# Kernel optimization log

Measured on AMD Instinct MI355X. Metric: run time of the kernel, lower is better.

The kernel has to match this reference:

```python
import jax, jax.numpy as jnp
import numpy as np

B, C, H, W = 2, 64, 128, 128

def setup_inputs() -> dict:
    key = jax.random.key(0)
    k1, k2, k3 = jax.random.split(key, 3)
    x = jax.random.normal(k1, (B, C, H, W), dtype=jnp.float32)
    y = jax.random.normal(k2, (B, C, H, W), dtype=jnp.float32)
    z = jax.random.normal(k3, (B, C, H, W), dtype=jnp.float32)
    return {"x": x, "y": y, "z": z}

def reference(x, y, z):
    # x=q, y=k, z=v, all [b,c,h,w]. Per pixel:
    #   kv[i,j] = v[i] * k[j]          (c x c outer product)
    #   attn    = softmax over i (dim=1 in torch, the v axis)
    #   out[i]  = sum_j attn[i,j] * q[j]
    q = jnp.transpose(x, (0, 2, 3, 1))  # [b,h,w,c]
    k = jnp.transpose(y, (0, 2, 3, 1))
    v = jnp.transpose(z, (0, 2, 3, 1))
    kv = v[..., :, None] * k[..., None, :]          # [b,h,w,c,c]
    attn = jax.nn.softmax(kv, axis=-2)              # softmax over v-axis i
    out = jnp.einsum('bhwij,bhwj->bhwi', attn, q)   # [b,h,w,c]
    return jnp.transpose(out, (0, 3, 1, 2))         # [b,c,h,w]
```

## Files before the change

kernel.cpp:

```cpp
#include <hip/hip_runtime.h>


constexpr int C    = 64;
constexpr int HW   = 128 * 128;
constexpr int NPIX = 2 * HW;
constexpr int ICH  = 8;
constexpr int JT   = 8;
constexpr int LSTR = 68;
#define LOG2E 1.4426950408889634f

__device__ __forceinline__ float quad_xor1_add(float x) {
  int xi = __builtin_bit_cast(int, x);
  int yi = __builtin_amdgcn_update_dpp(0, xi, 0xB1, 0xF, 0xF, true);
  return x + __builtin_bit_cast(float, yi);
}
__device__ __forceinline__ float quad_xor2_add(float x) {
  int xi = __builtin_bit_cast(int, x);
  int yi = __builtin_amdgcn_update_dpp(0, xi, 0x4E, 0xF, 0xF, true);
  return x + __builtin_bit_cast(float, yi);
}
__device__ __forceinline__ float xor4_add(float x) {
  int xi = __builtin_bit_cast(int, x);
  int yi = __builtin_amdgcn_ds_swizzle(xi, 0x101F);
  return x + __builtin_bit_cast(float, yi);
}

__global__ __launch_bounds__(256, 4) void channel_mixing_kernel(
    const float* __restrict__ q,
    const float* __restrict__ kk,
    const float* __restrict__ v,
    float* __restrict__ out) {
  __shared__ __align__(16) float lds_k[32 * LSTR];
  __shared__ __align__(16) float lds_q[32 * LSTR];

  const int t        = threadIdx.x;
  const int pixblock = blockIdx.x * 32;
  const int gbase = ((pixblock >> 14) << 20) | (pixblock & (HW - 1));

#pragma unroll
  for (int rep = 0; rep < 8; ++rep) {
    const int idx = rep * 256 + t;
    const int j   = idx >> 5;
    const int px  = idx & 31;
    lds_k[px * LSTR + j] = kk[gbase + (j << 14) + px];
    lds_q[px * LSTR + j] = q [gbase + (j << 14) + px];
  }

  const int lane = t & 63;
  const int p    = lane >> 3;
  const int ig   = lane & 7;
  const int px   = (t >> 6) * 8 + p;
  const int base  = gbase + px;
  const int cbase = base + (ig << 17);

  float vv[ICH];
#pragma unroll
  for (int ii = 0; ii < ICH; ++ii)
    vv[ii] = v[cbase + (ii << 14)] * LOG2E;

  float acc[ICH];
#pragma unroll
  for (int ii = 0; ii < ICH; ++ii) acc[ii] = 0.0f;

  __syncthreads();

  const float* lkp = &lds_k[px * LSTR];
  const float* lqp = &lds_q[px * LSTR];

#pragma unroll 1
  for (int jt = 0; jt < C / JT; ++jt) {
    float kx[JT], qx[JT];
    *(float4*)&kx[0] = *(const float4*)&lkp[jt * JT];
    *(float4*)&kx[4] = *(const float4*)&lkp[jt * JT + 4];
    *(float4*)&qx[0] = *(const float4*)&lqp[jt * JT];
    *(float4*)&qx[4] = *(const float4*)&lqp[jt * JT + 4];

    float e[JT][ICH];
#pragma unroll
    for (int jj = 0; jj < JT; ++jj)
#pragma unroll
      for (int ii = 0; ii < ICH; ++ii)
        e[jj][ii] = __builtin_amdgcn_exp2f(vv[ii] * kx[jj]);

    float S[JT];
#pragma unroll
    for (int jj = 0; jj < JT; ++jj) {
      float s0 = (e[jj][0] + e[jj][1]) + (e[jj][2] + e[jj][3]);
      float s1 = (e[jj][4] + e[jj][5]) + (e[jj][6] + e[jj][7]);
      S[jj] = s0 + s1;
    }
#pragma unroll
    for (int jj = 0; jj < JT; ++jj) S[jj] = quad_xor1_add(S[jj]);
#pragma unroll
    for (int jj = 0; jj < JT; ++jj) S[jj] = quad_xor2_add(S[jj]);
#pragma unroll
    for (int jj = 0; jj < JT; ++jj) S[jj] = xor4_add(S[jj]);

#pragma unroll
    for (int jj = 0; jj < JT; ++jj) {
      const float w = qx[jj] * __builtin_amdgcn_rcpf(S[jj]);
#pragma unroll
      for (int ii = 0; ii < ICH; ++ii) acc[ii] += w * e[jj][ii];
    }
  }

#pragma unroll
  for (int ii = 0; ii < ICH; ++ii)
    out[cbase + (ii << 14)] = acc[ii];
}

extern "C" void kernel_launch(void* const* d_in, const int* in_sizes, int n_in,
                              void* d_out, int out_size, void* d_ws, size_t ws_size,
                              hipStream_t stream) {
  const float* q  = (const float*)d_in[0];
  const float* kk = (const float*)d_in[1];
  const float* v  = (const float*)d_in[2];
  float* out = (float*)d_out;

  dim3 grid(NPIX / 32);
  dim3 block(256);
  channel_mixing_kernel<<<grid, block, 0, stream>>>(q, kk, v, out);
}
```

Baseline: 92.90 us.

## Split each pixel across 16 lanes with 4 channels each, DPP-only reduction

Each pixel is now handled by 16 lanes owning 4 output channels each, instead of 8 lanes owning 8. Blocks cover 16 pixels, which doubles the grid, and the launch bound asks for 6 waves per SIMD. The softmax denominator reduction adds a fourth step and replaces the ds_swizzle with row_half_mirror and row_mirror DPP moves. The aim is lower register pressure and higher occupancy to hide exp latency, at the cost of more cross-lane reduction work and more repeated LDS reads per exp.

```diff
diff --git a/kernel.cpp b/kernel.cpp
--- a/kernel.cpp
+++ b/kernel.cpp
@@ -4,54 +4,46 @@
 constexpr int C    = 64;
 constexpr int HW   = 128 * 128;
 constexpr int NPIX = 2 * HW;
-constexpr int ICH  = 8;
+constexpr int ICH  = 4;
 constexpr int JT   = 8;
+constexpr int PXB  = 16;
 constexpr int LSTR = 68;
 #define LOG2E 1.4426950408889634f
 
-__device__ __forceinline__ float quad_xor1_add(float x) {
+template <int CTRL>
+__device__ __forceinline__ float dpp_add(float x) {
   int xi = __builtin_bit_cast(int, x);
-  int yi = __builtin_amdgcn_update_dpp(0, xi, 0xB1, 0xF, 0xF, true);
-  return x + __builtin_bit_cast(float, yi);
-}
-__device__ __forceinline__ float quad_xor2_add(float x) {
-  int xi = __builtin_bit_cast(int, x);
-  int yi = __builtin_amdgcn_update_dpp(0, xi, 0x4E, 0xF, 0xF, true);
-  return x + __builtin_bit_cast(float, yi);
-}
-__device__ __forceinline__ float xor4_add(float x) {
-  int xi = __builtin_bit_cast(int, x);
-  int yi = __builtin_amdgcn_ds_swizzle(xi, 0x101F);
+  int yi = __builtin_amdgcn_update_dpp(0, xi, CTRL, 0xF, 0xF, true);
   return x + __builtin_bit_cast(float, yi);
 }
 
-__global__ __launch_bounds__(256, 4) void channel_mixing_kernel(
+__global__ __launch_bounds__(256, 6) void channel_mixing_kernel(
     const float* __restrict__ q,
     const float* __restrict__ kk,
     const float* __restrict__ v,
     float* __restrict__ out) {
-  __shared__ __align__(16) float lds_k[32 * LSTR];
-  __shared__ __align__(16) float lds_q[32 * LSTR];
+  __shared__ __align__(16) float lds_k[PXB * LSTR];
+  __shared__ __align__(16) float lds_q[PXB * LSTR];
 
   const int t        = threadIdx.x;
-  const int pixblock = blockIdx.x * 32;
+  const int pixblock = blockIdx.x * PXB;
   const int gbase = ((pixblock >> 14) << 20) | (pixblock & (HW - 1));
 
 #pragma unroll
-  for (int rep = 0; rep < 8; ++rep) {
+  for (int rep = 0; rep < 4; ++rep) {
     const int idx = rep * 256 + t;
-    const int j   = idx >> 5;
-    const int px  = idx & 31;
-    lds_k[px * LSTR + j] = kk[gbase + (j << 14) + px];
-    lds_q[px * LSTR + j] = q [gbase + (j << 14) + px];
+    const int j   = idx >> 4;
+    const int pxs = idx & 15;
+    lds_k[pxs * LSTR + j] = kk[gbase + (j << 14) + pxs];
+    lds_q[pxs * LSTR + j] = q [gbase + (j << 14) + pxs];
   }
 
   const int lane = t & 63;
-  const int p    = lane >> 3;
-  const int ig   = lane & 7;
-  const int px   = (t >> 6) * 8 + p;
+  const int p    = lane >> 4;
+  const int ig   = lane & 15;
+  const int px   = (t >> 6) * 4 + p;
   const int base  = gbase + px;
-  const int cbase = base + (ig << 17);
+  const int cbase = base + (ig << 16);
 
   float vv[ICH];
 #pragma unroll
@@ -84,17 +76,16 @@
 
     float S[JT];
 #pragma unroll
-    for (int jj = 0; jj < JT; ++jj) {
-      float s0 = (e[jj][0] + e[jj][1]) + (e[jj][2] + e[jj][3]);
-      float s1 = (e[jj][4] + e[jj][5]) + (e[jj][6] + e[jj][7]);
-      S[jj] = s0 + s1;
-    }
+    for (int jj = 0; jj < JT; ++jj)
+      S[jj] = (e[jj][0] + e[jj][1]) + (e[jj][2] + e[jj][3]);
 #pragma unroll
-    for (int jj = 0; jj < JT; ++jj) S[jj] = quad_xor1_add(S[jj]);
+    for (int jj = 0; jj < JT; ++jj) S[jj] = dpp_add<0xB1>(S[jj]);
 #pragma unroll
-    for (int jj = 0; jj < JT; ++jj) S[jj] = quad_xor2_add(S[jj]);
+    for (int jj = 0; jj < JT; ++jj) S[jj] = dpp_add<0x4E>(S[jj]);
 #pragma unroll
-    for (int jj = 0; jj < JT; ++jj) S[jj] = xor4_add(S[jj]);
+    for (int jj = 0; jj < JT; ++jj) S[jj] = dpp_add<0x141>(S[jj]);
+#pragma unroll
+    for (int jj = 0; jj < JT; ++jj) S[jj] = dpp_add<0x140>(S[jj]);
 
 #pragma unroll
     for (int jj = 0; jj < JT; ++jj) {
@@ -117,7 +108,7 @@
   const float* v  = (const float*)d_in[2];
   float* out = (float*)d_out;
 
-  dim3 grid(NPIX / 32);
+  dim3 grid(NPIX / PXB);
   dim3 block(256);
   channel_mixing_kernel<<<grid, block, 0, stream>>>(q, kk, v, out);
 }
```

After: 96.04 us. 3.4% more time.
